# Performance work log

Measured on AMD Instinct MI355X. Metric: run time of the kernel, lower is better.

## Reference

```python
import jax, jax.numpy as jnp
import numpy as np

G = 60            # 60x60 macroblock MV grid (960px / 16px blocks)
IMAGE_SIZE = 960.0
LN_EPS = 1e-5


def layer_norm(x, g, b):
    mu = jnp.mean(x, -1, keepdims=True)
    var = jnp.var(x, -1, keepdims=True)
    return (x - mu) / jnp.sqrt(var + LN_EPS) * g + b


def setup_inputs() -> dict:
    key = jax.random.key(0)
    ks = iter(jax.random.split(key, 40))
    nk = lambda: next(ks)
    N = 4096
    MVF, BED, H = 64, 32, 128
    D_IN = MVF + BED  # 96

    def lin(out_d, in_d):
        w = jax.random.normal(nk(), (out_d, in_d), jnp.float32) * np.float32(1.0 / np.sqrt(in_d))
        b = jnp.zeros((out_d,), jnp.float32)
        return w, b

    motion_vectors = jax.random.normal(nk(), (1, 2, G, G), jnp.float32)
    xy = jax.random.uniform(nk(), (N, 2), jnp.float32, 0.0, 800.0)
    wh = jax.random.uniform(nk(), (N, 2), jnp.float32, 16.0, 160.0)
    boxes = jnp.concatenate([xy, jnp.clip(xy + wh, 0.0, IMAGE_SIZE)], axis=-1)

    inp = {"motion_vectors": motion_vectors, "boxes": boxes}
    # stats projection: 6 stats (mean/std/range x 2 channels) -> MVF
    inp["W_stats"], inp["b_stats"] = lin(MVF, 6)
    inp["g_stats"] = jnp.ones((MVF,), jnp.float32); inp["be_stats"] = jnp.zeros((MVF,), jnp.float32)
    # box coordinate encoder
    inp["W_b1"], inp["b_b1"] = lin(BED, 4)
    inp["g_b1"] = jnp.ones((BED,), jnp.float32); inp["be_b1"] = jnp.zeros((BED,), jnp.float32)
    inp["W_b2"], inp["b_b2"] = lin(BED, BED)
    inp["g_b2"] = jnp.ones((BED,), jnp.float32); inp["be_b2"] = jnp.zeros((BED,), jnp.float32)
    # single-layer LSTM (torch gate order i,f,g,o)
    inp["W_ih"] = jax.random.normal(nk(), (4 * H, D_IN), jnp.float32) * np.float32(1.0 / np.sqrt(D_IN))
    inp["W_hh"] = jax.random.normal(nk(), (4 * H, H), jnp.float32) * np.float32(1.0 / np.sqrt(H))
    inp["b_ih"] = jnp.zeros((4 * H,), jnp.float32)
    inp["b_hh"] = jnp.zeros((4 * H,), jnp.float32)
    # heads
    inp["W_p1"], inp["b_p1"] = lin(H // 2, H); inp["W_p2"], inp["b_p2"] = lin(2, H // 2)
    inp["W_s1"], inp["b_s1"] = lin(H // 2, H); inp["W_s2"], inp["b_s2"] = lin(2, H // 2)
    inp["W_c1"], inp["b_c1"] = lin(H // 2, H); inp["W_c2"], inp["b_c2"] = lin(1, H // 2)
    return inp


def _box_motion_stats(motion_vectors, boxes_norm):
    # motion_vectors: [1,2,G,G]; boxes_norm: [N,4] in [0,1]
    mvf = motion_vectors[0].reshape(2, G * G)  # [2, 3600]
    x1 = jnp.clip(jnp.floor(boxes_norm[:, 0] * G).astype(jnp.int32), 0, G - 1)
    y1 = jnp.clip(jnp.floor(boxes_norm[:, 1] * G).astype(jnp.int32), 0, G - 1)
    x2 = jnp.clip(jnp.ceil(boxes_norm[:, 2] * G).astype(jnp.int32), x1 + 1, G)
    y2 = jnp.clip(jnp.ceil(boxes_norm[:, 3] * G).astype(jnp.int32), y1 + 1, G)
    idx = jnp.arange(G)
    mx = (idx[None, :] >= x1[:, None]) & (idx[None, :] < x2[:, None])  # [N,G]
    my = (idx[None, :] >= y1[:, None]) & (idx[None, :] < y2[:, None])  # [N,G]
    mask = (my[:, :, None] & mx[:, None, :]).reshape(-1, G * G).astype(mvf.dtype)  # [N,3600]
    cnt = mask.sum(-1, keepdims=True)  # >= 1 by construction
    s = jnp.einsum('nc,kc->nk', mask, mvf)          # [N,2]
    sq = jnp.einsum('nc,kc->nk', mask, mvf * mvf)   # [N,2]
    mean = s / cnt
    std = jnp.sqrt(jnp.clip(sq / cnt - mean * mean, 0.0))
    big = jnp.asarray(1e30, mvf.dtype)
    hi = jnp.where(mask[:, None, :] > 0, mvf[None], -big).max(-1)  # [N,2]
    lo = jnp.where(mask[:, None, :] > 0, mvf[None], big).min(-1)   # [N,2]
    return jnp.concatenate([mean, std, hi - lo], axis=-1)  # [N,6]


def reference(motion_vectors, boxes,
              W_stats, b_stats, g_stats, be_stats,
              W_b1, b_b1, g_b1, be_b1, W_b2, b_b2, g_b2, be_b2,
              W_ih, W_hh, b_ih, b_hh,
              W_p1, b_p1, W_p2, b_p2, W_s1, b_s1, W_s2, b_s2, W_c1, b_c1, W_c2, b_c2):
    N = boxes.shape[0]
    H = W_hh.shape[1]
    boxes_norm = jnp.clip(boxes / IMAGE_SIZE, 0.0, 1.0)

    # per-box motion feature (BoxAlignedMotionEncoder: gather region -> mean/std/range -> proj)
    stats = _box_motion_stats(motion_vectors, boxes_norm)
    mv_feat = jax.nn.relu(layer_norm(stats @ W_stats.T + b_stats, g_stats, be_stats))  # [N,64]

    # box coordinate encoder (dropout = identity in eval)
    h1 = jax.nn.relu(layer_norm(boxes_norm @ W_b1.T + b_b1, g_b1, be_b1))
    box_feat = jax.nn.relu(layer_norm(h1 @ W_b2.T + b_b2, g_b2, be_b2))  # [N,32]

    x = jnp.concatenate([mv_feat, box_feat], axis=-1)  # [N,96]

    # single-step LSTM, zero initial state, torch gate order i,f,g,o
    h0 = jnp.zeros((N, H), x.dtype)
    c0 = jnp.zeros((N, H), x.dtype)
    gates = x @ W_ih.T + h0 @ W_hh.T + b_ih + b_hh
    i, f, g, o = jnp.split(gates, 4, axis=-1)
    c = jax.nn.sigmoid(f) * c0 + jax.nn.sigmoid(i) * jnp.tanh(g)
    h = jax.nn.sigmoid(o) * jnp.tanh(c)  # [N,128]

    pos = jax.nn.relu(h @ W_p1.T + b_p1) @ W_p2.T + b_p2    # [N,2]
    size = jax.nn.relu(h @ W_s1.T + b_s1) @ W_s2.T + b_s2   # [N,2]
    conf = jax.nn.relu(h @ W_c1.T + b_c1) @ W_c2.T + b_c2   # [N,1]
    confidences = jax.nn.sigmoid(conf[:, 0])

    # box update: shift center by deltas, scale w/h by exp(size_deltas)
    x1, y1, x2, y2 = boxes[:, 0], boxes[:, 1], boxes[:, 2], boxes[:, 3]
    cx, cy = (x1 + x2) * 0.5, (y1 + y2) * 0.5
    w, hgt = x2 - x1, y2 - y1
    ncx, ncy = cx + pos[:, 0], cy + pos[:, 1]
    nw, nh = w * jnp.exp(size[:, 0]), hgt * jnp.exp(size[:, 1])
    pred = jnp.stack([ncx - nw * 0.5, ncy - nh * 0.5, ncx + nw * 0.5, ncy + nh * 0.5], axis=-1)
    return jnp.concatenate([pred, confidences[:, None]], axis=-1)  # [N,5]
```

## Files before the change

### kernel.cpp

```cpp
#include <hip/hip_runtime.h>
#include <math.h>

#define GRID_G 60
#define GRID_GG 3600
#define BPB 8

__device__ __forceinline__ float wred32sum(float v){
  #pragma unroll
  for (int m = 16; m; m >>= 1) v += __shfl_xor(v, m, 32);
  return v;
}
__device__ __forceinline__ float wred32max(float v){
  #pragma unroll
  for (int m = 16; m; m >>= 1) v = fmaxf(v, __shfl_xor(v, m, 32));
  return v;
}
__device__ __forceinline__ float wred32min(float v){
  #pragma unroll
  for (int m = 16; m; m >>= 1) v = fminf(v, __shfl_xor(v, m, 32));
  return v;
}
__device__ __forceinline__ float frcp(float x){ return __builtin_amdgcn_rcpf(x); }
__device__ __forceinline__ float fsig(float x){ return frcp(1.0f + __expf(-x)); }
__device__ __forceinline__ float ftanh(float x){ return 1.0f - 2.0f*frcp(1.0f + __expf(2.0f*x)); }

__global__ __launch_bounds__(256) void transpose_kernel(
    const float* __restrict__ W_ih,
    const float* __restrict__ W_p1, const float* __restrict__ W_s1,
    const float* __restrict__ W_c1,
    float* __restrict__ wt_ih, float* __restrict__ wt_h)
{
  const int i = blockIdx.x * 256 + threadIdx.x;
  if (i < 96*384) {
    const int k = i / 384, r = i % 384;
    const int row = (r < 128) ? r : (r + 128);
    wt_ih[i] = W_ih[row * 96 + k];
  } else {
    const int j = i - 96*384;
    if (j < 128*192) {
      const int k = j / 192, r = j % 192;
      const float* W = (r < 64) ? W_p1 : (r < 128) ? W_s1 : W_c1;
      wt_h[j] = W[(r & 63) * 128 + k];
    }
  }
}

__global__ __launch_bounds__(256) void tracker_kernel(
    const float* __restrict__ mv,
    const float* __restrict__ boxes,
    const float* __restrict__ W_stats, const float* __restrict__ b_stats,
    const float* __restrict__ g_stats, const float* __restrict__ be_stats,
    const float* __restrict__ W_b1,  const float* __restrict__ b_b1,
    const float* __restrict__ g_b1,  const float* __restrict__ be_b1,
    const float* __restrict__ W_b2,  const float* __restrict__ b_b2,
    const float* __restrict__ g_b2,  const float* __restrict__ be_b2,
    const float* __restrict__ wt_ih,
    const float* __restrict__ b_ih,  const float* __restrict__ b_hh,
    const float* __restrict__ wt_h,
    const float* __restrict__ b_p1,  const float* __restrict__ W_p2, const float* __restrict__ b_p2,
    const float* __restrict__ b_s1,  const float* __restrict__ W_s2, const float* __restrict__ b_s2,
    const float* __restrict__ b_c1,  const float* __restrict__ W_c2, const float* __restrict__ b_c2,
    float* __restrict__ out, int N)
{
  __shared__ __align__(16) float x_lds[BPB][96];
  __shared__ __align__(16) float gates_lds[BPB][384];
  __shared__ __align__(16) float h_lds[BPB][128];
  __shared__ __align__(16) float h1_lds[BPB][32];
  __shared__ float u_lds[3*BPB][65];
  __shared__ float res_lds[BPB][5];

  const int tid  = threadIdx.x;
  const int base = blockIdx.x * BPB;

  {
    const int b   = tid >> 5;
    const int l32 = tid & 31;
    int gb = base + b; if (gb >= N) gb = N - 1;
    const float4 bx = ((const float4*)boxes)[gb];
    const float bn0 = fminf(fmaxf(bx.x * (1.0f/960.0f), 0.f), 1.f);
    const float bn1 = fminf(fmaxf(bx.y * (1.0f/960.0f), 0.f), 1.f);
    const float bn2 = fminf(fmaxf(bx.z * (1.0f/960.0f), 0.f), 1.f);
    const float bn3 = fminf(fmaxf(bx.w * (1.0f/960.0f), 0.f), 1.f);

    int x1 = (int)floorf(bn0 * 60.f); x1 = min(max(x1, 0), 59);
    int y1 = (int)floorf(bn1 * 60.f); y1 = min(max(y1, 0), 59);
    int x2 = (int)ceilf (bn2 * 60.f); x2 = min(max(x2, x1 + 1), 60);
    int y2 = (int)ceilf (bn3 * 60.f); y2 = min(max(y2, y1 + 1), 60);
    const int w = x2 - x1, hh = y2 - y1;
    const int cnt = w * hh;
    const float rw = 1.0f / (float)w;

    float s0=0.f, s1=0.f, q0=0.f, q1=0.f;
    float hi0=-1e30f, hi1=-1e30f, lo0=1e30f, lo1=1e30f;
    for (int c = l32; c < cnt; c += 32) {
      const int yy = (int)(((float)c + 0.5f) * rw);
      const int xx = c - yy * w;
      const int idx = (y1 + yy) * GRID_G + (x1 + xx);
      const float m0 = mv[idx];
      const float m1 = mv[GRID_GG + idx];
      s0 += m0; q0 += m0*m0; hi0 = fmaxf(hi0, m0); lo0 = fminf(lo0, m0);
      s1 += m1; q1 += m1*m1; hi1 = fmaxf(hi1, m1); lo1 = fminf(lo1, m1);
    }
    s0 = wred32sum(s0); q0 = wred32sum(q0); hi0 = wred32max(hi0); lo0 = wred32min(lo0);
    s1 = wred32sum(s1); q1 = wred32sum(q1); hi1 = wred32max(hi1); lo1 = wred32min(lo1);
    const float inv = frcp((float)cnt);
    float st[6];
    st[0] = s0 * inv;
    st[1] = s1 * inv;
    st[2] = sqrtf(fmaxf(q0 * inv - st[0]*st[0], 0.f));
    st[3] = sqrtf(fmaxf(q1 * inv - st[1]*st[1], 0.f));
    st[4] = hi0 - lo0;
    st[5] = hi1 - lo1;

    {
      const float* Wr0 = W_stats + l32 * 6;
      const float* Wr1 = W_stats + (l32 + 32) * 6;
      float v0 = b_stats[l32], v1 = b_stats[l32 + 32];
      #pragma unroll
      for (int k = 0; k < 6; ++k) { v0 = fmaf(st[k], Wr0[k], v0); v1 = fmaf(st[k], Wr1[k], v1); }
      const float mu  = wred32sum(v0 + v1) * (1.0f/64.0f);
      const float var = wred32sum(v0*v0 + v1*v1) * (1.0f/64.0f) - mu*mu;
      const float rs  = rsqrtf(var + 1e-5f);
      x_lds[b][l32     ] = fmaxf((v0-mu)*rs*g_stats[l32     ] + be_stats[l32     ], 0.f);
      x_lds[b][l32 + 32] = fmaxf((v1-mu)*rs*g_stats[l32 + 32] + be_stats[l32 + 32], 0.f);
    }

    {
      const float* Wr = W_b1 + l32 * 4;
      const float v = b_b1[l32] + bn0*Wr[0] + bn1*Wr[1] + bn2*Wr[2] + bn3*Wr[3];
      const float mu  = wred32sum(v)   * (1.0f/32.0f);
      const float var = wred32sum(v*v) * (1.0f/32.0f) - mu*mu;
      h1_lds[b][l32] = fmaxf((v - mu) * rsqrtf(var + 1e-5f) * g_b1[l32] + be_b1[l32], 0.f);
    }
    __threadfence_block();

    {
      const float* Wr = W_b2 + l32 * 32;
      float v = b_b2[l32];
      #pragma unroll
      for (int kk = 0; kk < 8; ++kk) {
        const float4 hv = *(const float4*)(&h1_lds[b][kk * 4]);
        const float4 wv = *(const float4*)(&Wr[kk * 4]);
        v = fmaf(wv.x,hv.x, fmaf(wv.y,hv.y, fmaf(wv.z,hv.z, fmaf(wv.w,hv.w, v))));
      }
      const float mu  = wred32sum(v)   * (1.0f/32.0f);
      const float var = wred32sum(v*v) * (1.0f/32.0f) - mu*mu;
      x_lds[b][64 + l32] = fmaxf((v - mu) * rsqrtf(var + 1e-5f) * g_b2[l32] + be_b2[l32], 0.f);
    }
  }
  __syncthreads();

  if (tid < 192) {
    const int g = (tid < 96) ? tid : tid - 96;
    const int s = (tid < 96) ? 0 : 1;
    const int bs = s * 4;
    float acc[4][4];
    #pragma unroll
    for (int b = 0; b < 4; ++b)
      #pragma unroll
      for (int j = 0; j < 4; ++j) acc[b][j] = 0.f;
    const float4* WT = (const float4*)wt_ih;
    #pragma unroll 2
    for (int k4 = 0; k4 < 24; ++k4) {
      float4 wv[4];
      #pragma unroll
      for (int kk = 0; kk < 4; ++kk) wv[kk] = WT[(size_t)(4*k4 + kk) * 96 + g];
      float4 xv[4];
      #pragma unroll
      for (int b = 0; b < 4; ++b) xv[b] = *(const float4*)(&x_lds[bs + b][k4 * 4]);
      #pragma unroll
      for (int b = 0; b < 4; ++b) {
        acc[b][0] = fmaf(wv[0].x, xv[b].x, fmaf(wv[1].x, xv[b].y, fmaf(wv[2].x, xv[b].z, fmaf(wv[3].x, xv[b].w, acc[b][0]))));
        acc[b][1] = fmaf(wv[0].y, xv[b].x, fmaf(wv[1].y, xv[b].y, fmaf(wv[2].y, xv[b].z, fmaf(wv[3].y, xv[b].w, acc[b][1]))));
        acc[b][2] = fmaf(wv[0].z, xv[b].x, fmaf(wv[1].z, xv[b].y, fmaf(wv[2].z, xv[b].z, fmaf(wv[3].z, xv[b].w, acc[b][2]))));
        acc[b][3] = fmaf(wv[0].w, xv[b].x, fmaf(wv[1].w, xv[b].y, fmaf(wv[2].w, xv[b].z, fmaf(wv[3].w, xv[b].w, acc[b][3]))));
      }
    }
    #pragma unroll
    for (int b = 0; b < 4; ++b)
      #pragma unroll
      for (int j = 0; j < 4; ++j)
        gates_lds[bs + b][4*g + j] = acc[b][j];
  }
  __syncthreads();

  {
    const int j    = tid & 127;
    const int half = tid >> 7;
    const float bi = b_ih[j      ] + b_hh[j      ];
    const float bg = b_ih[j + 256] + b_hh[j + 256];
    const float bo = b_ih[j + 384] + b_hh[j + 384];
    #pragma unroll
    for (int bb = 0; bb < 4; ++bb) {
      const int b = half * 4 + bb;
      const float ai = gates_lds[b][j      ] + bi;
      const float ag = gates_lds[b][128 + j] + bg;
      const float ao = gates_lds[b][256 + j] + bo;
      const float c  = fsig(ai) * ftanh(ag);
      h_lds[b][j] = fsig(ao) * ftanh(c);
    }
  }
  __syncthreads();

  if (tid < 192) {
    const int s   = tid / 48;
    const int g48 = tid - s * 48;
    const int bs  = s * 2;
    float acc[2][4];
    #pragma unroll
    for (int b = 0; b < 2; ++b)
      #pragma unroll
      for (int j = 0; j < 4; ++j) acc[b][j] = 0.f;
    const float4* WT = (const float4*)wt_h;
    #pragma unroll 2
    for (int k4 = 0; k4 < 32; ++k4) {
      float4 wv[4];
      #pragma unroll
      for (int kk = 0; kk < 4; ++kk) wv[kk] = WT[(size_t)(4*k4 + kk) * 48 + g48];
      float4 hv[2];
      #pragma unroll
      for (int b = 0; b < 2; ++b) hv[b] = *(const float4*)(&h_lds[bs + b][k4 * 4]);
      #pragma unroll
      for (int b = 0; b < 2; ++b) {
        acc[b][0] = fmaf(wv[0].x, hv[b].x, fmaf(wv[1].x, hv[b].y, fmaf(wv[2].x, hv[b].z, fmaf(wv[3].x, hv[b].w, acc[b][0]))));
        acc[b][1] = fmaf(wv[0].y, hv[b].x, fmaf(wv[1].y, hv[b].y, fmaf(wv[2].y, hv[b].z, fmaf(wv[3].y, hv[b].w, acc[b][1]))));
        acc[b][2] = fmaf(wv[0].z, hv[b].x, fmaf(wv[1].z, hv[b].y, fmaf(wv[2].z, hv[b].z, fmaf(wv[3].z, hv[b].w, acc[b][2]))));
        acc[b][3] = fmaf(wv[0].w, hv[b].x, fmaf(wv[1].w, hv[b].y, fmaf(wv[2].w, hv[b].z, fmaf(wv[3].w, hv[b].w, acc[b][3]))));
      }
    }
    const int r0   = 4 * g48;
    const int head = r0 >> 6;
    const int brow = r0 & 63;
    const float* B1 = (head == 0) ? b_p1 : (head == 1) ? b_s1 : b_c1;
    #pragma unroll
    for (int j = 0; j < 4; ++j) {
      const float bias = B1[brow + j];
      #pragma unroll
      for (int b = 0; b < 2; ++b)
        u_lds[head * BPB + bs + b][brow + j] = fmaxf(acc[b][j] + bias, 0.f);
    }
  }
  __syncthreads();

  if (tid < BPB * 5) {
    const int b = tid / 5, o = tid % 5;
    const int head = (o < 2) ? 0 : (o < 4) ? 1 : 2;
    const float* W2; float bias;
    if      (o == 0) { W2 = W_p2;      bias = b_p2[0]; }
    else if (o == 1) { W2 = W_p2 + 64; bias = b_p2[1]; }
    else if (o == 2) { W2 = W_s2;      bias = b_s2[0]; }
    else if (o == 3) { W2 = W_s2 + 64; bias = b_s2[1]; }
    else             { W2 = W_c2;      bias = b_c2[0]; }
    const float* ur = u_lds[head * BPB + b];
    float a0 = bias, a1 = 0.f, a2 = 0.f, a3 = 0.f;
    #pragma unroll 4
    for (int k = 0; k < 64; k += 4) {
      a0 = fmaf(ur[k  ], W2[k  ], a0);
      a1 = fmaf(ur[k+1], W2[k+1], a1);
      a2 = fmaf(ur[k+2], W2[k+2], a2);
      a3 = fmaf(ur[k+3], W2[k+3], a3);
    }
    res_lds[b][o] = (a0 + a1) + (a2 + a3);
  }
  __syncthreads();

  if (tid < BPB) {
    const int gb = base + tid;
    if (gb < N) {
      const float4 bx = ((const float4*)boxes)[gb];
      const float cx = (bx.x + bx.z) * 0.5f;
      const float cy = (bx.y + bx.w) * 0.5f;
      const float w  = bx.z - bx.x;
      const float hh = bx.w - bx.y;
      const float ncx = cx + res_lds[tid][0];
      const float ncy = cy + res_lds[tid][1];
      const float nw  = w  * __expf(res_lds[tid][2]);
      const float nh  = hh * __expf(res_lds[tid][3]);
      const float cf  = fsig(res_lds[tid][4]);
      float* op = out + (size_t)gb * 5;
      op[0] = ncx - nw * 0.5f;
      op[1] = ncy - nh * 0.5f;
      op[2] = ncx + nw * 0.5f;
      op[3] = ncy + nh * 0.5f;
      op[4] = cf;
    }
  }
}

extern "C" void kernel_launch(void* const* d_in, const int* in_sizes, int n_in,
                              void* d_out, int out_size, void* d_ws, size_t ws_size,
                              hipStream_t stream) {
  (void)n_in; (void)out_size; (void)ws_size;
  const float* mv       = (const float*)d_in[0];
  const float* boxes    = (const float*)d_in[1];
  const float* W_stats  = (const float*)d_in[2];
  const float* b_stats  = (const float*)d_in[3];
  const float* g_stats  = (const float*)d_in[4];
  const float* be_stats = (const float*)d_in[5];
  const float* W_b1     = (const float*)d_in[6];
  const float* b_b1     = (const float*)d_in[7];
  const float* g_b1     = (const float*)d_in[8];
  const float* be_b1    = (const float*)d_in[9];
  const float* W_b2     = (const float*)d_in[10];
  const float* b_b2     = (const float*)d_in[11];
  const float* g_b2     = (const float*)d_in[12];
  const float* be_b2    = (const float*)d_in[13];
  const float* W_ih     = (const float*)d_in[14];
  const float* b_ih     = (const float*)d_in[16];
  const float* b_hh     = (const float*)d_in[17];
  const float* W_p1     = (const float*)d_in[18];
  const float* b_p1     = (const float*)d_in[19];
  const float* W_p2     = (const float*)d_in[20];
  const float* b_p2     = (const float*)d_in[21];
  const float* W_s1     = (const float*)d_in[22];
  const float* b_s1     = (const float*)d_in[23];
  const float* W_s2     = (const float*)d_in[24];
  const float* b_s2     = (const float*)d_in[25];
  const float* W_c1     = (const float*)d_in[26];
  const float* b_c1     = (const float*)d_in[27];
  const float* W_c2     = (const float*)d_in[28];
  const float* b_c2     = (const float*)d_in[29];

  float* wt_ih = (float*)d_ws;
  float* wt_h  = wt_ih + 96 * 384;

  transpose_kernel<<<240, 256, 0, stream>>>(W_ih, W_p1, W_s1, W_c1, wt_ih, wt_h);

  const int N = in_sizes[1] / 4;
  const int grid = (N + BPB - 1) / BPB;
  tracker_kernel<<<grid, 256, 0, stream>>>(
      mv, boxes,
      W_stats, b_stats, g_stats, be_stats,
      W_b1, b_b1, g_b1, be_b1,
      W_b2, b_b2, g_b2, be_b2,
      wt_ih, b_ih, b_hh,
      wt_h,
      b_p1, W_p2, b_p2,
      b_s1, W_s2, b_s2,
      b_c1, W_c2, b_c2,
      (float*)d_out, N);
}
```

Measured before the change: 132.6 us.

## Split GEMV reductions along K so each weight load serves all 8 boxes

The LSTM input projection and the head first-layer GEMVs now split the reduction dimension K across thread groups instead of splitting the batch. Each thread reuses its loaded weight float4s across all 8 boxes in the block, which halves or quarters global weight traffic per block. Partial sums go to two new LDS buffers and are combined in the activation step and in a new reduction pass, at the cost of more LDS, an extra barrier and more accumulator registers. The weight-transpose kernel is also changed to write float4 outputs with a quarter of the blocks.

```diff
diff --git a/kernel.cpp b/kernel.cpp
--- a/kernel.cpp
+++ b/kernel.cpp
@@ -30,18 +30,29 @@
     const float* __restrict__ W_c1,
     float* __restrict__ wt_ih, float* __restrict__ wt_h)
 {
-  const int i = blockIdx.x * 256 + threadIdx.x;
-  if (i < 96*384) {
-    const int k = i / 384, r = i % 384;
-    const int row = (r < 128) ? r : (r + 128);
-    wt_ih[i] = W_ih[row * 96 + k];
-  } else {
-    const int j = i - 96*384;
-    if (j < 128*192) {
-      const int k = j / 192, r = j % 192;
-      const float* W = (r < 64) ? W_p1 : (r < 128) ? W_s1 : W_c1;
-      wt_h[j] = W[(r & 63) * 128 + k];
-    }
+  const int i4 = blockIdx.x * 256 + threadIdx.x;
+  if (i4 < 9216) {
+    const int e = i4 * 4;
+    const int k = e / 384, r0 = e % 384;
+    float4 v;
+    {
+      const int r = r0;     const int row = (r < 128) ? r : r + 128; v.x = W_ih[row*96 + k];
+    }
+    { const int r = r0 + 1; const int row = (r < 128) ? r : r + 128; v.y = W_ih[row*96 + k]; }
+    { const int r = r0 + 2; const int row = (r < 128) ? r : r + 128; v.z = W_ih[row*96 + k]; }
+    { const int r = r0 + 3; const int row = (r < 128) ? r : r + 128; v.w = W_ih[row*96 + k]; }
+    ((float4*)wt_ih)[i4] = v;
+  } else if (i4 < 9216 + 6144) {
+    const int j4 = i4 - 9216;
+    const int e = j4 * 4;
+    const int k = e / 192, r0 = e % 192;
+    const float* W = (r0 < 64) ? W_p1 : (r0 < 128) ? W_s1 : W_c1;
+    float4 v;
+    v.x = W[((r0    ) & 63) * 128 + k];
+    v.y = W[((r0 + 1) & 63) * 128 + k];
+    v.z = W[((r0 + 2) & 63) * 128 + k];
+    v.w = W[((r0 + 3) & 63) * 128 + k];
+    ((float4*)wt_h)[j4] = v;
   }
 }
 
@@ -63,7 +74,8 @@
     float* __restrict__ out, int N)
 {
   __shared__ __align__(16) float x_lds[BPB][96];
-  __shared__ __align__(16) float gates_lds[BPB][384];
+  __shared__ __align__(16) float sA[BPB][384];
+  __shared__ __align__(16) float sB[BPB][384];
   __shared__ __align__(16) float h_lds[BPB][128];
   __shared__ __align__(16) float h1_lds[BPB][32];
   __shared__ float u_lds[3*BPB][65];
@@ -151,36 +163,37 @@
   __syncthreads();
 
   if (tid < 192) {
-    const int g = (tid < 96) ? tid : tid - 96;
+    const int q = (tid < 96) ? tid : tid - 96;
     const int s = (tid < 96) ? 0 : 1;
-    const int bs = s * 4;
-    float acc[4][4];
-    #pragma unroll
-    for (int b = 0; b < 4; ++b)
-      #pragma unroll
-      for (int j = 0; j < 4; ++j) acc[b][j] = 0.f;
+    float acc[4][BPB];
+    #pragma unroll
+    for (int j = 0; j < 4; ++j)
+      #pragma unroll
+      for (int b = 0; b < BPB; ++b) acc[j][b] = 0.f;
     const float4* WT = (const float4*)wt_ih;
+    const int k0 = s * 48;
     #pragma unroll 2
-    for (int k4 = 0; k4 < 24; ++k4) {
-      float4 wv[4];
-      #pragma unroll
-      for (int kk = 0; kk < 4; ++kk) wv[kk] = WT[(size_t)(4*k4 + kk) * 96 + g];
-      float4 xv[4];
-      #pragma unroll
-      for (int b = 0; b < 4; ++b) xv[b] = *(const float4*)(&x_lds[bs + b][k4 * 4]);
-      #pragma unroll
-      for (int b = 0; b < 4; ++b) {
-        acc[b][0] = fmaf(wv[0].x, xv[b].x, fmaf(wv[1].x, xv[b].y, fmaf(wv[2].x, xv[b].z, fmaf(wv[3].x, xv[b].w, acc[b][0]))));
-        acc[b][1] = fmaf(wv[0].y, xv[b].x, fmaf(wv[1].y, xv[b].y, fmaf(wv[2].y, xv[b].z, fmaf(wv[3].y, xv[b].w, acc[b][1]))));
-        acc[b][2] = fmaf(wv[0].z, xv[b].x, fmaf(wv[1].z, xv[b].y, fmaf(wv[2].z, xv[b].z, fmaf(wv[3].z, xv[b].w, acc[b][2]))));
-        acc[b][3] = fmaf(wv[0].w, xv[b].x, fmaf(wv[1].w, xv[b].y, fmaf(wv[2].w, xv[b].z, fmaf(wv[3].w, xv[b].w, acc[b][3]))));
+    for (int k4 = 0; k4 < 12; ++k4) {
+      const int kb = k0 + 4*k4;
+      const float4 wv0 = WT[(size_t)(kb    ) * 96 + q];
+      const float4 wv1 = WT[(size_t)(kb + 1) * 96 + q];
+      const float4 wv2 = WT[(size_t)(kb + 2) * 96 + q];
+      const float4 wv3 = WT[(size_t)(kb + 3) * 96 + q];
+      #pragma unroll
+      for (int b = 0; b < BPB; ++b) {
+        const float4 xv = *(const float4*)(&x_lds[b][kb]);
+        acc[0][b] = fmaf(wv0.x, xv.x, fmaf(wv1.x, xv.y, fmaf(wv2.x, xv.z, fmaf(wv3.x, xv.w, acc[0][b]))));
+        acc[1][b] = fmaf(wv0.y, xv.x, fmaf(wv1.y, xv.y, fmaf(wv2.y, xv.z, fmaf(wv3.y, xv.w, acc[1][b]))));
+        acc[2][b] = fmaf(wv0.z, xv.x, fmaf(wv1.z, xv.y, fmaf(wv2.z, xv.z, fmaf(wv3.z, xv.w, acc[2][b]))));
+        acc[3][b] = fmaf(wv0.w, xv.x, fmaf(wv1.w, xv.y, fmaf(wv2.w, xv.z, fmaf(wv3.w, xv.w, acc[3][b]))));
       }
     }
-    #pragma unroll
-    for (int b = 0; b < 4; ++b)
-      #pragma unroll
-      for (int j = 0; j < 4; ++j)
-        gates_lds[bs + b][4*g + j] = acc[b][j];
+    float* dst = (s == 0) ? &sA[0][0] : &sB[0][0];
+    #pragma unroll
+    for (int b = 0; b < BPB; ++b) {
+      float4 v; v.x = acc[0][b]; v.y = acc[1][b]; v.z = acc[2][b]; v.w = acc[3][b];
+      *(float4*)(dst + b * 384 + 4 * q) = v;
+    }
   }
   __syncthreads();
 
@@ -193,9 +206,9 @@
     #pragma unroll
     for (int bb = 0; bb < 4; ++bb) {
       const int b = half * 4 + bb;
-      const float ai = gates_lds[b][j      ] + bi;
-      const float ag = gates_lds[b][128 + j] + bg;
-      const float ao = gates_lds[b][256 + j] + bo;
+      const float ai = sA[b][j      ] + sB[b][j      ] + bi;
+      const float ag = sA[b][128 + j] + sB[b][128 + j] + bg;
+      const float ao = sA[b][256 + j] + sB[b][256 + j] + bo;
       const float c  = fsig(ai) * ftanh(ag);
       h_lds[b][j] = fsig(ao) * ftanh(c);
     }
@@ -203,41 +216,51 @@
   __syncthreads();
 
   if (tid < 192) {
-    const int s   = tid / 48;
-    const int g48 = tid - s * 48;
-    const int bs  = s * 2;
-    float acc[2][4];
-    #pragma unroll
-    for (int b = 0; b < 2; ++b)
-      #pragma unroll
-      for (int j = 0; j < 4; ++j) acc[b][j] = 0.f;
+    const int q48 = tid % 48;
+    const int s4  = tid / 48;
+    float acc[4][BPB];
+    #pragma unroll
+    for (int j = 0; j < 4; ++j)
+      #pragma unroll
+      for (int b = 0; b < BPB; ++b) acc[j][b] = 0.f;
     const float4* WT = (const float4*)wt_h;
+    const int k0 = s4 * 32;
     #pragma unroll 2
-    for (int k4 = 0; k4 < 32; ++k4) {
-      float4 wv[4];
-      #pragma unroll
-      for (int kk = 0; kk < 4; ++kk) wv[kk] = WT[(size_t)(4*k4 + kk) * 48 + g48];
-      float4 hv[2];
-      #pragma unroll
-      for (int b = 0; b < 2; ++b) hv[b] = *(const float4*)(&h_lds[bs + b][k4 * 4]);
-      #pragma unroll
-      for (int b = 0; b < 2; ++b) {
-        acc[b][0] = fmaf(wv[0].x, hv[b].x, fmaf(wv[1].x, hv[b].y, fmaf(wv[2].x, hv[b].z, fmaf(wv[3].x, hv[b].w, acc[b][0]))));
-        acc[b][1] = fmaf(wv[0].y, hv[b].x, fmaf(wv[1].y, hv[b].y, fmaf(wv[2].y, hv[b].z, fmaf(wv[3].y, hv[b].w, acc[b][1]))));
-        acc[b][2] = fmaf(wv[0].z, hv[b].x, fmaf(wv[1].z, hv[b].y, fmaf(wv[2].z, hv[b].z, fmaf(wv[3].z, hv[b].w, acc[b][2]))));
-        acc[b][3] = fmaf(wv[0].w, hv[b].x, fmaf(wv[1].w, hv[b].y, fmaf(wv[2].w, hv[b].z, fmaf(wv[3].w, hv[b].w, acc[b][3]))));
+    for (int k4 = 0; k4 < 8; ++k4) {
+      const int kb = k0 + 4*k4;
+      const float4 wv0 = WT[(size_t)(kb    ) * 48 + q48];
+      const float4 wv1 = WT[(size_t)(kb + 1) * 48 + q48];
+      const float4 wv2 = WT[(size_t)(kb + 2) * 48 + q48];
+      const float4 wv3 = WT[(size_t)(kb + 3) * 48 + q48];
+      #pragma unroll
+      for (int b = 0; b < BPB; ++b) {
+        const float4 hv = *(const float4*)(&h_lds[b][kb]);
+        acc[0][b] = fmaf(wv0.x, hv.x, fmaf(wv1.x, hv.y, fmaf(wv2.x, hv.z, fmaf(wv3.x, hv.w, acc[0][b]))));
+        acc[1][b] = fmaf(wv0.y, hv.x, fmaf(wv1.y, hv.y, fmaf(wv2.y, hv.z, fmaf(wv3.y, hv.w, acc[1][b]))));
+        acc[2][b] = fmaf(wv0.z, hv.x, fmaf(wv1.z, hv.y, fmaf(wv2.z, hv.z, fmaf(wv3.z, hv.w, acc[2][b]))));
+        acc[3][b] = fmaf(wv0.w, hv.x, fmaf(wv1.w, hv.y, fmaf(wv2.w, hv.z, fmaf(wv3.w, hv.w, acc[3][b]))));
       }
     }
-    const int r0   = 4 * g48;
-    const int head = r0 >> 6;
-    const int brow = r0 & 63;
-    const float* B1 = (head == 0) ? b_p1 : (head == 1) ? b_s1 : b_c1;
-    #pragma unroll
-    for (int j = 0; j < 4; ++j) {
-      const float bias = B1[brow + j];
-      #pragma unroll
-      for (int b = 0; b < 2; ++b)
-        u_lds[head * BPB + bs + b][brow + j] = fmaxf(acc[b][j] + bias, 0.f);
+    float* dst = (s4 < 2) ? &sA[0][0] : &sB[0][0];
+    const int off = (s4 & 1) * 192;
+    #pragma unroll
+    for (int b = 0; b < BPB; ++b) {
+      float4 v; v.x = acc[0][b]; v.y = acc[1][b]; v.z = acc[2][b]; v.w = acc[3][b];
+      *(float4*)(dst + b * 384 + off + 4 * q48) = v;
+    }
+  }
+  __syncthreads();
+
+  {
+    #pragma unroll
+    for (int i = 0; i < 6; ++i) {
+      const int idx = tid + 256 * i;
+      const int b = idx / 192;
+      const int r = idx - b * 192;
+      const int head = r >> 6, brow = r & 63;
+      const float bias = ((head == 0) ? b_p1 : (head == 1) ? b_s1 : b_c1)[brow];
+      const float v = sA[b][r] + sA[b][192 + r] + sB[b][r] + sB[b][192 + r] + bias;
+      u_lds[head * BPB + b][brow] = fmaxf(v, 0.f);
     }
   }
   __syncthreads();
@@ -324,7 +347,7 @@
   float* wt_ih = (float*)d_ws;
   float* wt_h  = wt_ih + 96 * 384;
 
-  transpose_kernel<<<240, 256, 0, stream>>>(W_ih, W_p1, W_s1, W_c1, wt_ih, wt_h);
+  transpose_kernel<<<60, 256, 0, stream>>>(W_ih, W_p1, W_s1, W_c1, wt_ih, wt_h);
 
   const int N = in_sizes[1] / 4;
   const int grid = (N + BPB - 1) / BPB;
```

Measured after the change: 131.5 us. Within noise of the previous version (-0.8%).
